# Kernel optimization log

Measured on AMD Instinct MI355X. Metric: run time of the kernel, lower is better.

## Reference

```python
import jax, jax.numpy as jnp
import numpy as np

N_QUBITS = 10
U3_LAYERS = 2
ENT_LAYERS = 2
EDGES = [[(q, (q + 1) % N_QUBITS) for q in range(N_QUBITS)] for _ in range(ENT_LAYERS)]
FIXED_W = [np.zeros(N_QUBITS, dtype=np.float32) for _ in range(ENT_LAYERS)]
C64 = jnp.complex64


def _rz(a):
    a = a.astype(C64)
    em, ep = jnp.exp(-0.5j * a), jnp.exp(0.5j * a)
    z = jnp.zeros((), C64)
    return jnp.stack([jnp.stack([em, z]), jnp.stack([z, ep])])


def _ry(t):
    c = jnp.cos(t / 2).astype(C64)
    s = jnp.sin(t / 2).astype(C64)
    return jnp.stack([jnp.stack([c, -s]), jnp.stack([s, c])])


def _rot(phi, theta, omega):
    # PennyLane Rot = RZ(omega) @ RY(theta) @ RZ(phi)
    return _rz(omega) @ _ry(theta) @ _rz(phi)


def _apply_1q(state, U, q):
    # state: (B,) + (2,)*n ; apply 2x2 U on qubit axis 1+q
    s = jnp.moveaxis(state, 1 + q, -1)
    s = s @ U.T
    return jnp.moveaxis(s, -1, 1 + q)


def _apply_cry(state, theta, u, v):
    U = _ry(theta)
    s = jnp.moveaxis(state, (1 + u, 1 + v), (-2, -1))  # (..., ctrl, tgt)
    c0 = s[..., 0, :]
    c1 = s[..., 1, :] @ U.T
    s = jnp.stack([c0, c1], axis=-2)
    return jnp.moveaxis(s, (-2, -1), (1 + u, 1 + v))


def _circuit(inputs, weights):
    B = inputs.shape[0]
    n = N_QUBITS
    # invert=True -> angles = pi * clamp(x, 0, 1)
    ang = jnp.pi * jnp.clip(inputs, 0.0, 1.0)
    # AngleEmbedding RY on |0...0> gives a product state
    c = jnp.cos(ang / 2).astype(C64)
    s = jnp.sin(ang / 2).astype(C64)
    st = jnp.ones((B, 1), C64)
    for q in range(n):
        amp = jnp.stack([c[:, q], s[:, q]], axis=-1)  # (B, 2)
        st = (st[:, :, None] * amp[:, None, :]).reshape(B, -1)
    st = st.reshape((B,) + (2,) * n)  # axis 1+q == wire q

    w_idx = 0
    for L in range(max(U3_LAYERS, ENT_LAYERS)):
        if L < U3_LAYERS:
            for q in range(n):
                U = _rot(weights[w_idx], weights[w_idx + 1], weights[w_idx + 2])
                w_idx += 3
                st = _apply_1q(st, U, q)
        if L < ENT_LAYERS:
            fw = FIXED_W[L]
            for i, (u, v) in enumerate(EDGES[L]):
                th = weights[w_idx] + fw[i]
                w_idx += 1
                st = _apply_cry(st, th, u, v)

    probs = (st.real ** 2 + st.imag ** 2)  # (B,) + (2,)*n
    outs = []
    for q in range(n):
        axes = tuple(a for a in range(1, n + 1) if a != 1 + q)
        m = jnp.sum(probs, axis=axes)  # (B, 2)
        outs.append(m[:, 0] - m[:, 1])
    return jnp.stack(outs, axis=-1)  # (B, n)


def setup_inputs() -> dict:
    key = jax.random.key(0)
    k1, k2 = jax.random.split(key)
    inputs = jax.random.uniform(k1, (8192, N_QUBITS), dtype=jnp.float32)
    weights = 0.1 * jax.random.normal(k2, (80,), dtype=jnp.float32)
    return {"inputs": inputs, "weights": weights}


def reference(inputs, weights):
    return _circuit(inputs, weights)
```

## Files before the change

kernel.cpp:

```cpp
#include <hip/hip_runtime.h>
#include <math.h>

#define NQ 10
typedef float v2f __attribute__((ext_vector_type(2)));

#define RL(v, l) __int_as_float(__builtin_amdgcn_readlane(__float_as_int(v), (l)))

template<int CTRL>
__device__ __forceinline__ float dppf(float x) {
    return __int_as_float(__builtin_amdgcn_update_dpp(
        __float_as_int(x), __float_as_int(x), CTRL, 0xF, 0xF, true));
}
template<int OFS>
__device__ __forceinline__ float swzf(float x) {
    return __int_as_float(__builtin_amdgcn_ds_swizzle(__float_as_int(x), OFS));
}
__device__ __forceinline__ float bperm(int idx, float x) {
    return __int_as_float(__builtin_amdgcn_ds_bpermute(idx, __float_as_int(x)));
}

template<int P>
__device__ __forceinline__ float partner1(float x, int bpx32) {
    if constexpr (P == 0) return dppf<0xB1>(x);
    else if constexpr (P == 1) return dppf<0x4E>(x);
    else if constexpr (P == 2) return swzf<0x101F>(x);
    else if constexpr (P == 3) return dppf<0x128>(x);
    else if constexpr (P == 4) return swzf<0x401F>(x);
    else return bperm(bpx32, x);
}
template<int P>
__device__ __forceinline__ v2f partner2(v2f v, int bpx32) {
    v2f r;
    r.x = partner1<P>(v.x, bpx32);
    r.y = partner1<P>(v.y, bpx32);
    return r;
}

__device__ __forceinline__ void u3_pair(v2f& a0r, v2f& a0i, v2f& a1r, v2f& a1i,
                                        float u00r, float u00i, float u01r, float u01i,
                                        float u10r, float u10i, float u11r, float u11i) {
    v2f n0r = u00r * a0r - u00i * a0i + u01r * a1r - u01i * a1i;
    v2f n0i = u00r * a0i + u00i * a0r + u01r * a1i + u01i * a1r;
    v2f n1r = u10r * a0r - u10i * a0i + u11r * a1r - u11i * a1i;
    v2f n1i = u10r * a0i + u10i * a0r + u11r * a1i + u11i * a1r;
    a0r = n0r; a0i = n0i; a1r = n1r; a1i = n1i;
}
__device__ __forceinline__ void ry_pair(v2f& a0r, v2f& a0i, v2f& a1r, v2f& a1i,
                                        float c, float s) {
    v2f n0r = c * a0r - s * a1r;
    v2f n0i = c * a0i - s * a1i;
    v2f n1r = s * a0r + c * a1r;
    v2f n1i = s * a0i + c * a1i;
    a0r = n0r; a0i = n0i; a1r = n1r; a1i = n1i;
}

template<int P>
__device__ __forceinline__ void u3_lane(v2f (&Sr)[8], v2f (&Si)[8], int lane, int bpx32,
                                        float u00r, float u00i, float u01r, float u01i,
                                        float u10r, float u10i, float u11r, float u11i) {
    const bool hi = (lane >> P) & 1;
    const float dr = hi ? u11r : u00r, di = hi ? u11i : u00i;
    const float orr = hi ? u10r : u01r, oii = hi ? u10i : u01i;
#pragma unroll
    for (int k = 0; k < 8; ++k) {
        const v2f mr = Sr[k], mi = Si[k];
        const v2f pr = partner2<P>(mr, bpx32);
        const v2f pi = partner2<P>(mi, bpx32);
        Sr[k] = dr * mr - di * mi + orr * pr - oii * pi;
        Si[k] = dr * mi + di * mr + orr * pi + oii * pr;
    }
}

template<int PC, int PT>
__device__ __forceinline__ void cry_lane(v2f (&Sr)[8], v2f (&Si)[8], int lane, int bpx32,
                                         float c, float s) {
    const bool ctrl = (lane >> PC) & 1;
    const float cl = ctrl ? c : 1.0f;
    const float sl = ctrl ? s : 0.0f;
    const bool hi = (lane >> PT) & 1;
    const float sgn = hi ? sl : -sl;
#pragma unroll
    for (int k = 0; k < 8; ++k) {
        const v2f pr = partner2<PT>(Sr[k], bpx32);
        const v2f pi = partner2<PT>(Si[k], bpx32);
        Sr[k] = cl * Sr[k] + sgn * pr;
        Si[k] = cl * Si[k] + sgn * pi;
    }
}

__device__ __forceinline__ float wave_sum(float x, int bpx32) {
    x += dppf<0xB1>(x);
    x += dppf<0x4E>(x);
    x += swzf<0x101F>(x);
    x += dppf<0x128>(x);
    x += swzf<0x401F>(x);
    x += bperm(bpx32, x);
    return x;
}

__global__ __launch_bounds__(256) void qsim(const float* __restrict__ in,
                                            const float* __restrict__ w,
                                            float* __restrict__ out, int B) {
    const int lane = threadIdx.x & 63;
    const int wave = threadIdx.x >> 6;
    int b = blockIdx.x * 4 + wave;
    b = __builtin_amdgcn_readfirstlane(b);
    if (b >= B) return;
    const int bpx32 = (lane ^ 32) << 2;

    float ang0 = 0.0f, ang1 = 0.0f, ang2 = 0.0f;
    if (lane < 20) {
        const int L = lane / 10, q = lane - L * 10;
        const int wi = L * 40 + q * 3;
        const float phi = w[wi], theta = w[wi + 1], omega = w[wi + 2];
        ang0 = 0.5f * theta;
        ang1 = 0.5f * (phi + omega);
        ang2 = 0.5f * (phi - omega);
    } else if (lane < 40) {
        const int g = lane - 20;
        const int L = g / 10, e = g - L * 10;
        ang0 = 0.5f * w[L * 40 + 30 + e];
    } else if (lane < 50) {
        float x = in[b * NQ + (lane - 40)];
        x = fminf(fmaxf(x, 0.0f), 1.0f);
        ang0 = 0.5f * 3.14159265358979323846f * x;
    }
    const float ca = __cosf(ang0), sa = __sinf(ang0);
    const float cb = __cosf(ang1), sb = __sinf(ang1);
    const float cg = __cosf(ang2), sg = __sinf(ang2);
    float c0, c1, c2, c3, c4, c5, c6, c7;
    c0 =  ca * cb;  c1 = -ca * sb;
    c2 = -sa * cg;  c3 = -sa * sg;
    c4 =  sa * cg;  c5 = -sa * sg;
    c6 =  ca * cb;  c7 =  ca * sb;
    if (lane >= 20) { c0 = ca; c1 = sa; }

#define U3C(L, q) \
    const float u00r = RL(c0, (L)*10+(q)), u00i = RL(c1, (L)*10+(q)), \
                u01r = RL(c2, (L)*10+(q)), u01i = RL(c3, (L)*10+(q)), \
                u10r = RL(c4, (L)*10+(q)), u10i = RL(c5, (L)*10+(q)), \
                u11r = RL(c6, (L)*10+(q)), u11i = RL(c7, (L)*10+(q));
#define CRYC(L, e) \
    const float c = RL(c0, 20+(L)*10+(e)), s = RL(c1, 20+(L)*10+(e));

    float cc[NQ], ss[NQ];
#pragma unroll
    for (int q = 0; q < NQ; ++q) { cc[q] = RL(c0, 40 + q); ss[q] = RL(c1, 40 + q); }
    float lamp = 1.0f;
#pragma unroll
    for (int j = 0; j < 6; ++j) lamp *= ((lane >> j) & 1) ? ss[9 - j] : cc[9 - j];

    v2f Sr[8], Si[8];
#pragma unroll
    for (int k = 0; k < 8; ++k) {
        float f = lamp;
        f *= (k & 1) ? ss[3] : cc[3];
        f *= (k & 2) ? ss[2] : cc[2];
        f *= (k & 4) ? ss[1] : cc[1];
        Sr[k] = (v2f){f * cc[0], f * ss[0]};
        Si[k] = (v2f){0.0f, 0.0f};
    }

#pragma unroll
    for (int L = 0; L < 2; ++L) {
        {
            U3C(L, 0);
            const v2f Dr = {u00r, u11r}, Di = {u00i, u11i};
            const v2f Or = {u01r, u10r}, Oi = {u01i, u10i};
#pragma unroll
            for (int k = 0; k < 8; ++k) {
                const v2f Ar = Sr[k], Ai = Si[k];
                const v2f Br = Ar.yx, Bi = Ai.yx;
                Sr[k] = Dr * Ar - Di * Ai + Or * Br - Oi * Bi;
                Si[k] = Dr * Ai + Di * Ar + Or * Bi + Oi * Br;
            }
        }
#pragma unroll
        for (int q = 1; q <= 3; ++q) {
            U3C(L, q);
            const int kb = (q == 1) ? 2 : (q == 2) ? 1 : 0;
            const int step = 1 << kb;
#pragma unroll
            for (int k0 = 0; k0 < 8; ++k0) {
                if (k0 & step) continue;
                const int k1 = k0 | step;
                u3_pair(Sr[k0], Si[k0], Sr[k1], Si[k1],
                        u00r, u00i, u01r, u01i, u10r, u10i, u11r, u11i);
            }
        }
        { U3C(L, 4); u3_lane<5>(Sr, Si, lane, bpx32, u00r,u00i,u01r,u01i,u10r,u10i,u11r,u11i); }
        { U3C(L, 5); u3_lane<4>(Sr, Si, lane, bpx32, u00r,u00i,u01r,u01i,u10r,u10i,u11r,u11i); }
        { U3C(L, 6); u3_lane<3>(Sr, Si, lane, bpx32, u00r,u00i,u01r,u01i,u10r,u10i,u11r,u11i); }
        { U3C(L, 7); u3_lane<2>(Sr, Si, lane, bpx32, u00r,u00i,u01r,u01i,u10r,u10i,u11r,u11i); }
        { U3C(L, 8); u3_lane<1>(Sr, Si, lane, bpx32, u00r,u00i,u01r,u01i,u10r,u10i,u11r,u11i); }
        { U3C(L, 9); u3_lane<0>(Sr, Si, lane, bpx32, u00r,u00i,u01r,u01i,u10r,u10i,u11r,u11i); }

        {
            CRYC(L, 0);
            const v2f cv = {1.0f, c};
            const v2f sv = {0.0f, s};
#pragma unroll
            for (int k0 = 0; k0 < 4; ++k0) {
                const int k1 = k0 | 4;
                v2f n0r = cv * Sr[k0] - sv * Sr[k1];
                v2f n0i = cv * Si[k0] - sv * Si[k1];
                v2f n1r = sv * Sr[k0] + cv * Sr[k1];
                v2f n1i = sv * Si[k0] + cv * Si[k1];
                Sr[k0] = n0r; Si[k0] = n0i; Sr[k1] = n1r; Si[k1] = n1i;
            }
        }
        {
            CRYC(L, 1);
            ry_pair(Sr[4], Si[4], Sr[6], Si[6], c, s);
            ry_pair(Sr[5], Si[5], Sr[7], Si[7], c, s);
        }
        {
            CRYC(L, 2);
            ry_pair(Sr[2], Si[2], Sr[3], Si[3], c, s);
            ry_pair(Sr[6], Si[6], Sr[7], Si[7], c, s);
        }
        {
            CRYC(L, 3);
            const bool hi = (lane >> 5) & 1;
            const float sgn = hi ? s : -s;
#pragma unroll
            for (int k = 1; k < 8; k += 2) {
                const v2f pr = partner2<5>(Sr[k], bpx32);
                const v2f pi = partner2<5>(Si[k], bpx32);
                Sr[k] = c * Sr[k] + sgn * pr;
                Si[k] = c * Si[k] + sgn * pi;
            }
        }
        { CRYC(L, 4); cry_lane<5, 4>(Sr, Si, lane, bpx32, c, s); }
        { CRYC(L, 5); cry_lane<4, 3>(Sr, Si, lane, bpx32, c, s); }
        { CRYC(L, 6); cry_lane<3, 2>(Sr, Si, lane, bpx32, c, s); }
        { CRYC(L, 7); cry_lane<2, 1>(Sr, Si, lane, bpx32, c, s); }
        { CRYC(L, 8); cry_lane<1, 0>(Sr, Si, lane, bpx32, c, s); }
        {
            CRYC(L, 9);
            const bool ctrl = lane & 1;
            const float cl = ctrl ? c : 1.0f;
            const float sl = ctrl ? s : 0.0f;
            const v2f C2 = {cl, cl};
            const v2f S2 = {-sl, sl};
#pragma unroll
            for (int k = 0; k < 8; ++k) {
                const v2f Ar = Sr[k], Ai = Si[k];
                Sr[k] = C2 * Ar + S2 * Ar.yx;
                Si[k] = C2 * Ai + S2 * Ai.yx;
            }
        }
    }

    v2f P[8];
    float ptot = 0.0f;
#pragma unroll
    for (int k = 0; k < 8; ++k) {
        P[k] = Sr[k] * Sr[k] + Si[k] * Si[k];
        ptot += P[k].x + P[k].y;
    }
    float z[NQ];
    {
        float acc = 0.0f;
#pragma unroll
        for (int k = 0; k < 8; ++k) acc += P[k].x - P[k].y;
        z[0] = acc;
    }
#pragma unroll
    for (int q = 1; q <= 3; ++q) {
        const int kb = (q == 1) ? 2 : (q == 2) ? 1 : 0;
        float acc = 0.0f;
#pragma unroll
        for (int k = 0; k < 8; ++k) {
            const float pk = P[k].x + P[k].y;
            acc += ((k >> kb) & 1) ? -pk : pk;
        }
        z[q] = acc;
    }
#pragma unroll
    for (int q = 4; q < NQ; ++q) {
        const int p = 9 - q;
        z[q] = ((lane >> p) & 1) ? -ptot : ptot;
    }
#pragma unroll
    for (int q = 0; q < NQ; ++q) z[q] = wave_sum(z[q], bpx32);

    if (lane == 0) {
#pragma unroll
        for (int q = 0; q < NQ; ++q) out[b * NQ + q] = z[q];
    }
}

extern "C" void kernel_launch(void* const* d_in, const int* in_sizes, int n_in,
                              void* d_out, int out_size, void* d_ws, size_t ws_size,
                              hipStream_t stream) {
    const float* inputs  = (const float*)d_in[0];
    const float* weights = (const float*)d_in[1];
    float* out = (float*)d_out;
    const int B = in_sizes[0] / NQ;

    qsim<<<(B + 3) / 4, 256, 0, stream>>>(inputs, weights, out, B);
}
```

Measured before the change: 96.66 us.

## Precompute fused gate matrices, fold embedding into first layer, use permlane swaps

A small precompute kernel builds the U3 matrices and fuses each CRY with the next U3 in the second layer into combined controlled matrices stored in workspace. The main kernel folds the embedding and first U3 layer into per-qubit single-qubit states, which removes the first-layer gate passes. Cross-half lane exchanges use permlane16/32 swap builtins when available. The Z-expectation reductions share a butterfly over the total probability. This adds a second kernel launch and workspace reads in exchange for fewer gate passes and fewer cross-lane ops.

Result: faster. 87.91 us (-9.0%).

```diff
diff --git a/kernel.cpp b/kernel.cpp
--- a/kernel.cpp
+++ b/kernel.cpp
@@ -4,7 +4,11 @@
 #define NQ 10
 typedef float v2f __attribute__((ext_vector_type(2)));
 
-#define RL(v, l) __int_as_float(__builtin_amdgcn_readlane(__float_as_int(v), (l)))
+#if defined(__has_builtin)
+#if __has_builtin(__builtin_amdgcn_permlane16_swap) && __has_builtin(__builtin_amdgcn_permlane32_swap)
+#define HAVE_PL 1
+#endif
+#endif
 
 template<int CTRL>
 __device__ __forceinline__ float dppf(float x) {
@@ -20,22 +24,100 @@
 }
 
 template<int P>
-__device__ __forceinline__ float partner1(float x, int bpx32) {
+__device__ __forceinline__ float partner1(float x) {
     if constexpr (P == 0) return dppf<0xB1>(x);
     else if constexpr (P == 1) return dppf<0x4E>(x);
     else if constexpr (P == 2) return swzf<0x101F>(x);
-    else if constexpr (P == 3) return dppf<0x128>(x);
-    else if constexpr (P == 4) return swzf<0x401F>(x);
-    else return bperm(bpx32, x);
-}
-template<int P>
-__device__ __forceinline__ v2f partner2(v2f v, int bpx32) {
-    v2f r;
-    r.x = partner1<P>(v.x, bpx32);
-    r.y = partner1<P>(v.y, bpx32);
-    return r;
-}
-
+    else return dppf<0x128>(x);
+}
+template<int P>
+__device__ __forceinline__ v2f partner2(v2f v) {
+    v2f r; r.x = partner1<P>(v.x); r.y = partner1<P>(v.y); return r;
+}
+
+struct FPair { float v0, v1; };
+template<int P>
+__device__ __forceinline__ FPair blkswap1(float x, int lane) {
+    FPair o;
+#ifdef HAVE_PL
+    if constexpr (P == 4) {
+        auto r = __builtin_amdgcn_permlane16_swap(__float_as_uint(x), __float_as_uint(x), false, false);
+        o.v0 = __uint_as_float(r[0]);
+        o.v1 = __uint_as_float(r[1]);
+    } else {
+        auto r = __builtin_amdgcn_permlane32_swap(__float_as_uint(x), __float_as_uint(x), false, false);
+        o.v0 = __uint_as_float(r[0]);
+        o.v1 = __uint_as_float(r[1]);
+    }
+#else
+    const float p = (P == 4) ? swzf<0x401F>(x) : bperm((lane ^ 32) << 2, x);
+    const bool hi = (lane >> P) & 1;
+    o.v0 = hi ? p : x;
+    o.v1 = hi ? x : p;
+#endif
+    return o;
+}
+struct VPair { v2f V0, V1; };
+template<int P>
+__device__ __forceinline__ VPair blkswap2(v2f x, int lane) {
+    const FPair a = blkswap1<P>(x.x, lane);
+    const FPair b = blkswap1<P>(x.y, lane);
+    VPair o;
+    o.V0 = (v2f){a.v0, b.v0};
+    o.V1 = (v2f){a.v1, b.v1};
+    return o;
+}
+template<int P>
+__device__ __forceinline__ float blkadd(float x, int lane) {
+    const FPair o = blkswap1<P>(x, lane);
+    return o.v0 + o.v1;
+}
+
+template<int P>
+__device__ __forceinline__ void gate_blk_full(v2f (&Sr)[8], v2f (&Si)[8], int lane,
+                                              float er, float ei, float fr, float fi) {
+#pragma unroll
+    for (int k = 0; k < 8; ++k) {
+        const VPair R = blkswap2<P>(Sr[k], lane);
+        const VPair I = blkswap2<P>(Si[k], lane);
+        Sr[k] = er * R.V0 - ei * I.V0 + fr * R.V1 - fi * I.V1;
+        Si[k] = er * I.V0 + ei * R.V0 + fr * I.V1 + fi * R.V1;
+    }
+}
+template<int P>
+__device__ __forceinline__ void gate_blk_real(v2f (&Sr)[8], v2f (&Si)[8], int lane,
+                                              float e, float f) {
+#pragma unroll
+    for (int k = 0; k < 8; ++k) {
+        const VPair R = blkswap2<P>(Sr[k], lane);
+        const VPair I = blkswap2<P>(Si[k], lane);
+        Sr[k] = e * R.V0 + f * R.V1;
+        Si[k] = e * I.V0 + f * I.V1;
+    }
+}
+template<int P>
+__device__ __forceinline__ void gate_dpp_full(v2f (&Sr)[8], v2f (&Si)[8],
+                                              float dr, float di, float orr, float oii) {
+#pragma unroll
+    for (int k = 0; k < 8; ++k) {
+        const v2f mr = Sr[k], mi = Si[k];
+        const v2f pr = partner2<P>(mr);
+        const v2f pi = partner2<P>(mi);
+        Sr[k] = dr * mr - di * mi + orr * pr - oii * pi;
+        Si[k] = dr * mi + di * mr + orr * pi + oii * pr;
+    }
+}
+template<int P>
+__device__ __forceinline__ void gate_dpp_real(v2f (&Sr)[8], v2f (&Si)[8],
+                                              float cl, float sgn) {
+#pragma unroll
+    for (int k = 0; k < 8; ++k) {
+        const v2f pr = partner2<P>(Sr[k]);
+        const v2f pi = partner2<P>(Si[k]);
+        Sr[k] = cl * Sr[k] + sgn * pr;
+        Si[k] = cl * Si[k] + sgn * pi;
+    }
+}
 __device__ __forceinline__ void u3_pair(v2f& a0r, v2f& a0i, v2f& a1r, v2f& a1i,
                                         float u00r, float u00i, float u01r, float u01i,
                                         float u10r, float u10i, float u11r, float u11i) {
@@ -53,237 +135,396 @@
     v2f n1i = s * a0i + c * a1i;
     a0r = n0r; a0i = n0i; a1r = n1r; a1i = n1i;
 }
-
-template<int P>
-__device__ __forceinline__ void u3_lane(v2f (&Sr)[8], v2f (&Si)[8], int lane, int bpx32,
-                                        float u00r, float u00i, float u01r, float u01i,
-                                        float u10r, float u10i, float u11r, float u11i) {
-    const bool hi = (lane >> P) & 1;
-    const float dr = hi ? u11r : u00r, di = hi ? u11i : u00i;
-    const float orr = hi ? u10r : u01r, oii = hi ? u10i : u01i;
-#pragma unroll
-    for (int k = 0; k < 8; ++k) {
-        const v2f mr = Sr[k], mi = Si[k];
-        const v2f pr = partner2<P>(mr, bpx32);
-        const v2f pi = partner2<P>(mi, bpx32);
-        Sr[k] = dr * mr - di * mi + orr * pr - oii * pi;
-        Si[k] = dr * mi + di * mr + orr * pi + oii * pr;
-    }
-}
-
-template<int PC, int PT>
-__device__ __forceinline__ void cry_lane(v2f (&Sr)[8], v2f (&Si)[8], int lane, int bpx32,
-                                         float c, float s) {
-    const bool ctrl = (lane >> PC) & 1;
-    const float cl = ctrl ? c : 1.0f;
-    const float sl = ctrl ? s : 0.0f;
-    const bool hi = (lane >> PT) & 1;
-    const float sgn = hi ? sl : -sl;
-#pragma unroll
-    for (int k = 0; k < 8; ++k) {
-        const v2f pr = partner2<PT>(Sr[k], bpx32);
-        const v2f pi = partner2<PT>(Si[k], bpx32);
-        Sr[k] = cl * Sr[k] + sgn * pr;
-        Si[k] = cl * Si[k] + sgn * pi;
-    }
-}
-
-__device__ __forceinline__ float wave_sum(float x, int bpx32) {
-    x += dppf<0xB1>(x);
-    x += dppf<0x4E>(x);
-    x += swzf<0x101F>(x);
-    x += dppf<0x128>(x);
-    x += swzf<0x401F>(x);
-    x += bperm(bpx32, x);
+__device__ __forceinline__ void cmul(float& xr, float& xi, float br, float bi) {
+    const float nr = xr * br - xi * bi;
+    const float ni = xr * bi + xi * br;
+    xr = nr; xi = ni;
+}
+
+template<int FROM>
+__device__ __forceinline__ float plus_reduce(float x, int lane) {
+    if constexpr (FROM <= 0) x += dppf<0xB1>(x);
+    if constexpr (FROM <= 1) x += dppf<0x4E>(x);
+    if constexpr (FROM <= 2) x += swzf<0x101F>(x);
+    if constexpr (FROM <= 3) x += dppf<0x128>(x);
+    if constexpr (FROM <= 4) x = blkadd<4>(x, lane);
+    x = blkadd<5>(x, lane);
     return x;
 }
 
+__device__ __forceinline__ void makeU3(float phi, float theta, float omega, float* u) {
+    const float ct = cosf(0.5f * theta), st = sinf(0.5f * theta);
+    const float apo = 0.5f * (phi + omega), amo = 0.5f * (phi - omega);
+    const float capo = cosf(apo), sapo = sinf(apo);
+    const float camo = cosf(amo), samo = sinf(amo);
+    u[0] =  capo * ct;  u[1] = -sapo * ct;
+    u[2] = -camo * st;  u[3] = -samo * st;
+    u[4] =  camo * st;  u[5] = -samo * st;
+    u[6] =  capo * ct;  u[7] =  sapo * ct;
+}
+
+__global__ void precompute(const float* __restrict__ w, float* __restrict__ cw) {
+    const int t = threadIdx.x;
+    if (t < 10) {
+        float u[8];
+        makeU3(w[t * 3], w[t * 3 + 1], w[t * 3 + 2], u);
+        float* p = cw + t * 8;
+        p[0] = u[0]; p[1] = u[2];
+        p[2] = u[1]; p[3] = u[3];
+        p[4] = u[4]; p[5] = u[6];
+        p[6] = u[5]; p[7] = u[7];
+    } else if (t < 20) {
+        const int q = t - 10;
+        float u[8];
+        makeU3(w[40 + q * 3], w[40 + q * 3 + 1], w[40 + q * 3 + 2], u);
+        float* p = cw + 100 + q * 8;
+        for (int i = 0; i < 8; ++i) p[i] = u[i];
+    } else if (t < 29) {
+        const int e = t - 20;
+        const float th = 0.5f * w[30 + e];
+        cw[80 + 2 * e] = cosf(th);
+        cw[81 + 2 * e] = sinf(th);
+    } else if (t == 29) {
+        const float th = 0.5f * w[79];
+        cw[98] = cosf(th);
+        cw[99] = sinf(th);
+    } else if (t < 40) {
+        const int q = t - 30;
+        float u[8];
+        makeU3(w[40 + q * 3], w[40 + q * 3 + 1], w[40 + q * 3 + 2], u);
+        float* p = cw + 180 + q * 8;
+        if (q == 0) {
+            const float th = 0.5f * w[39];
+            const float ct = cosf(th), st = sinf(th);
+            p[0] = u[0] * ct + u[2] * st;  p[1] = u[1] * ct + u[3] * st;
+            p[2] = u[2] * ct - u[0] * st;  p[3] = u[3] * ct - u[1] * st;
+            p[4] = u[4] * ct + u[6] * st;  p[5] = u[5] * ct + u[7] * st;
+            p[6] = u[6] * ct - u[4] * st;  p[7] = u[7] * ct - u[5] * st;
+        } else {
+            const float th = 0.5f * w[70 + (q - 1)];
+            const float ct = cosf(th), st = sinf(th);
+            p[0] = ct * u[0] - st * u[4];  p[1] = ct * u[1] - st * u[5];
+            p[2] = ct * u[2] - st * u[6];  p[3] = ct * u[3] - st * u[7];
+            p[4] = st * u[0] + ct * u[4];  p[5] = st * u[1] + ct * u[5];
+            p[6] = st * u[2] + ct * u[6];  p[7] = st * u[3] + ct * u[7];
+        }
+    }
+}
+
+#define LOADM(P, base) \
+    const float P##00r = cf[(base) + 0], P##00i = cf[(base) + 1], \
+                P##01r = cf[(base) + 2], P##01i = cf[(base) + 3], \
+                P##10r = cf[(base) + 4], P##10i = cf[(base) + 5], \
+                P##11r = cf[(base) + 6], P##11i = cf[(base) + 7];
+
 __global__ __launch_bounds__(256) void qsim(const float* __restrict__ in,
-                                            const float* __restrict__ w,
+                                            const float* __restrict__ cf,
                                             float* __restrict__ out, int B) {
+    __shared__ float tsh[4 * 40];
     const int lane = threadIdx.x & 63;
     const int wave = threadIdx.x >> 6;
     int b = blockIdx.x * 4 + wave;
     b = __builtin_amdgcn_readfirstlane(b);
     if (b >= B) return;
-    const int bpx32 = (lane ^ 32) << 2;
-
-    float ang0 = 0.0f, ang1 = 0.0f, ang2 = 0.0f;
-    if (lane < 20) {
-        const int L = lane / 10, q = lane - L * 10;
-        const int wi = L * 40 + q * 3;
-        const float phi = w[wi], theta = w[wi + 1], omega = w[wi + 2];
-        ang0 = 0.5f * theta;
-        ang1 = 0.5f * (phi + omega);
-        ang2 = 0.5f * (phi - omega);
-    } else if (lane < 40) {
-        const int g = lane - 20;
-        const int L = g / 10, e = g - L * 10;
-        ang0 = 0.5f * w[L * 40 + 30 + e];
-    } else if (lane < 50) {
-        float x = in[b * NQ + (lane - 40)];
+
+    if (lane < 40) {
+        const int q = lane >> 2;
+        float x = in[b * NQ + q];
         x = fminf(fmaxf(x, 0.0f), 1.0f);
-        ang0 = 0.5f * 3.14159265358979323846f * x;
-    }
-    const float ca = __cosf(ang0), sa = __sinf(ang0);
-    const float cb = __cosf(ang1), sb = __sinf(ang1);
-    const float cg = __cosf(ang2), sg = __sinf(ang2);
-    float c0, c1, c2, c3, c4, c5, c6, c7;
-    c0 =  ca * cb;  c1 = -ca * sb;
-    c2 = -sa * cg;  c3 = -sa * sg;
-    c4 =  sa * cg;  c5 = -sa * sg;
-    c6 =  ca * cb;  c7 =  ca * sb;
-    if (lane >= 20) { c0 = ca; c1 = sa; }
-
-#define U3C(L, q) \
-    const float u00r = RL(c0, (L)*10+(q)), u00i = RL(c1, (L)*10+(q)), \
-                u01r = RL(c2, (L)*10+(q)), u01i = RL(c3, (L)*10+(q)), \
-                u10r = RL(c4, (L)*10+(q)), u10i = RL(c5, (L)*10+(q)), \
-                u11r = RL(c6, (L)*10+(q)), u11i = RL(c7, (L)*10+(q));
-#define CRYC(L, e) \
-    const float c = RL(c0, 20+(L)*10+(e)), s = RL(c1, 20+(L)*10+(e));
-
-    float cc[NQ], ss[NQ];
-#pragma unroll
-    for (int q = 0; q < NQ; ++q) { cc[q] = RL(c0, 40 + q); ss[q] = RL(c1, 40 + q); }
-    float lamp = 1.0f;
-#pragma unroll
-    for (int j = 0; j < 6; ++j) lamp *= ((lane >> j) & 1) ? ss[9 - j] : cc[9 - j];
-
+        const float a = 0.5f * 3.14159265358979323846f * x;
+        const float ca = __cosf(a), sa = __sinf(a);
+        const float M0 = cf[lane * 2], M1 = cf[lane * 2 + 1];
+        tsh[wave * 40 + lane] = M0 * ca + M1 * sa;
+    }
+    const int base = wave * 40;
+
+    float wr, wi;
+    {
+        const int bit = lane & 1;
+        const float2 v = *(const float2*)&tsh[base + 9 * 4 + (bit << 1)];
+        wr = v.x; wi = v.y;
+    }
+#pragma unroll
+    for (int j = 1; j < 6; ++j) {
+        const int bit = (lane >> j) & 1;
+        const float2 v = *(const float2*)&tsh[base + (9 - j) * 4 + (bit << 1)];
+        cmul(wr, wi, v.x, v.y);
+    }
+    const float4 T0 = *(const float4*)&tsh[base + 0];
+    const float4 T1 = *(const float4*)&tsh[base + 4];
+    const float4 T2 = *(const float4*)&tsh[base + 8];
+    const float4 T3 = *(const float4*)&tsh[base + 12];
+
+    float vr[4], vi[4];
+    { float r = T1.x, i2 = T1.y; vr[0] = r * T2.x - i2 * T2.y; vi[0] = r * T2.y + i2 * T2.x;
+                                  vr[1] = r * T2.z - i2 * T2.w; vi[1] = r * T2.w + i2 * T2.z; }
+    { float r = T1.z, i2 = T1.w; vr[2] = r * T2.x - i2 * T2.y; vi[2] = r * T2.y + i2 * T2.x;
+                                  vr[3] = r * T2.z - i2 * T2.w; vi[3] = r * T2.w + i2 * T2.z; }
     v2f Sr[8], Si[8];
+    const v2f T0r = {T0.x, T0.z};
+    const v2f T0i = {T0.y, T0.w};
 #pragma unroll
     for (int k = 0; k < 8; ++k) {
-        float f = lamp;
-        f *= (k & 1) ? ss[3] : cc[3];
-        f *= (k & 2) ? ss[2] : cc[2];
-        f *= (k & 4) ? ss[1] : cc[1];
-        Sr[k] = (v2f){f * cc[0], f * ss[0]};
-        Si[k] = (v2f){0.0f, 0.0f};
-    }
-
-#pragma unroll
-    for (int L = 0; L < 2; ++L) {
-        {
-            U3C(L, 0);
-            const v2f Dr = {u00r, u11r}, Di = {u00i, u11i};
-            const v2f Or = {u01r, u10r}, Oi = {u01i, u10i};
-#pragma unroll
-            for (int k = 0; k < 8; ++k) {
-                const v2f Ar = Sr[k], Ai = Si[k];
-                const v2f Br = Ar.yx, Bi = Ai.yx;
-                Sr[k] = Dr * Ar - Di * Ai + Or * Br - Oi * Bi;
-                Si[k] = Dr * Ai + Di * Ar + Or * Bi + Oi * Br;
-            }
-        }
-#pragma unroll
-        for (int q = 1; q <= 3; ++q) {
-            U3C(L, q);
-            const int kb = (q == 1) ? 2 : (q == 2) ? 1 : 0;
-            const int step = 1 << kb;
-#pragma unroll
-            for (int k0 = 0; k0 < 8; ++k0) {
-                if (k0 & step) continue;
-                const int k1 = k0 | step;
-                u3_pair(Sr[k0], Si[k0], Sr[k1], Si[k1],
-                        u00r, u00i, u01r, u01i, u10r, u10i, u11r, u11i);
-            }
-        }
-        { U3C(L, 4); u3_lane<5>(Sr, Si, lane, bpx32, u00r,u00i,u01r,u01i,u10r,u10i,u11r,u11i); }
-        { U3C(L, 5); u3_lane<4>(Sr, Si, lane, bpx32, u00r,u00i,u01r,u01i,u10r,u10i,u11r,u11i); }
-        { U3C(L, 6); u3_lane<3>(Sr, Si, lane, bpx32, u00r,u00i,u01r,u01i,u10r,u10i,u11r,u11i); }
-        { U3C(L, 7); u3_lane<2>(Sr, Si, lane, bpx32, u00r,u00i,u01r,u01i,u10r,u10i,u11r,u11i); }
-        { U3C(L, 8); u3_lane<1>(Sr, Si, lane, bpx32, u00r,u00i,u01r,u01i,u10r,u10i,u11r,u11i); }
-        { U3C(L, 9); u3_lane<0>(Sr, Si, lane, bpx32, u00r,u00i,u01r,u01i,u10r,u10i,u11r,u11i); }
-
-        {
-            CRYC(L, 0);
-            const v2f cv = {1.0f, c};
-            const v2f sv = {0.0f, s};
-#pragma unroll
-            for (int k0 = 0; k0 < 4; ++k0) {
-                const int k1 = k0 | 4;
-                v2f n0r = cv * Sr[k0] - sv * Sr[k1];
-                v2f n0i = cv * Si[k0] - sv * Si[k1];
-                v2f n1r = sv * Sr[k0] + cv * Sr[k1];
-                v2f n1i = sv * Si[k0] + cv * Si[k1];
-                Sr[k0] = n0r; Si[k0] = n0i; Sr[k1] = n1r; Si[k1] = n1i;
-            }
-        }
-        {
-            CRYC(L, 1);
-            ry_pair(Sr[4], Si[4], Sr[6], Si[6], c, s);
-            ry_pair(Sr[5], Si[5], Sr[7], Si[7], c, s);
-        }
-        {
-            CRYC(L, 2);
-            ry_pair(Sr[2], Si[2], Sr[3], Si[3], c, s);
-            ry_pair(Sr[6], Si[6], Sr[7], Si[7], c, s);
-        }
-        {
-            CRYC(L, 3);
-            const bool hi = (lane >> 5) & 1;
-            const float sgn = hi ? s : -s;
-#pragma unroll
-            for (int k = 1; k < 8; k += 2) {
-                const v2f pr = partner2<5>(Sr[k], bpx32);
-                const v2f pi = partner2<5>(Si[k], bpx32);
-                Sr[k] = c * Sr[k] + sgn * pr;
-                Si[k] = c * Si[k] + sgn * pi;
-            }
-        }
-        { CRYC(L, 4); cry_lane<5, 4>(Sr, Si, lane, bpx32, c, s); }
-        { CRYC(L, 5); cry_lane<4, 3>(Sr, Si, lane, bpx32, c, s); }
-        { CRYC(L, 6); cry_lane<3, 2>(Sr, Si, lane, bpx32, c, s); }
-        { CRYC(L, 7); cry_lane<2, 1>(Sr, Si, lane, bpx32, c, s); }
-        { CRYC(L, 8); cry_lane<1, 0>(Sr, Si, lane, bpx32, c, s); }
-        {
-            CRYC(L, 9);
-            const bool ctrl = lane & 1;
-            const float cl = ctrl ? c : 1.0f;
-            const float sl = ctrl ? s : 0.0f;
-            const v2f C2 = {cl, cl};
-            const v2f S2 = {-sl, sl};
-#pragma unroll
-            for (int k = 0; k < 8; ++k) {
-                const v2f Ar = Sr[k], Ai = Si[k];
-                Sr[k] = C2 * Ar + S2 * Ar.yx;
-                Si[k] = C2 * Ai + S2 * Ai.yx;
-            }
+        const int hv = k >> 1;
+        const float t3r = (k & 1) ? T3.z : T3.x;
+        const float t3i = (k & 1) ? T3.w : T3.y;
+        float kr = vr[hv] * t3r - vi[hv] * t3i;
+        float ki = vr[hv] * t3i + vi[hv] * t3r;
+        cmul(kr, ki, wr, wi);
+        Sr[k] = kr * T0r - ki * T0i;
+        Si[k] = kr * T0i + ki * T0r;
+    }
+
+    {
+        const float c = cf[80], s = cf[81];
+        const v2f cv = {1.0f, c};
+        const v2f sv = {0.0f, s};
+#pragma unroll
+        for (int k0 = 0; k0 < 4; ++k0) {
+            const int k1 = k0 | 4;
+            v2f n0r = cv * Sr[k0] - sv * Sr[k1];
+            v2f n0i = cv * Si[k0] - sv * Si[k1];
+            v2f n1r = sv * Sr[k0] + cv * Sr[k1];
+            v2f n1i = sv * Si[k0] + cv * Si[k1];
+            Sr[k0] = n0r; Si[k0] = n0i; Sr[k1] = n1r; Si[k1] = n1i;
+        }
+    }
+    {
+        const float c = cf[82], s = cf[83];
+        ry_pair(Sr[4], Si[4], Sr[6], Si[6], c, s);
+        ry_pair(Sr[5], Si[5], Sr[7], Si[7], c, s);
+    }
+    {
+        const float c = cf[84], s = cf[85];
+        ry_pair(Sr[2], Si[2], Sr[3], Si[3], c, s);
+        ry_pair(Sr[6], Si[6], Sr[7], Si[7], c, s);
+    }
+    {
+        const float c = cf[86], s = cf[87];
+        const bool hi = (lane >> 5) & 1;
+        const float e = hi ? s : c;
+        const float f = hi ? c : -s;
+#pragma unroll
+        for (int k = 1; k < 8; k += 2) {
+            const VPair R = blkswap2<5>(Sr[k], lane);
+            const VPair I = blkswap2<5>(Si[k], lane);
+            Sr[k] = e * R.V0 + f * R.V1;
+            Si[k] = e * I.V0 + f * I.V1;
+        }
+    }
+    {
+        const float c = cf[88], s = cf[89];
+        const bool ctrl = (lane >> 5) & 1;
+        const bool hi = (lane >> 4) & 1;
+        const float e = ctrl ? (hi ? s : c) : (hi ? 0.0f : 1.0f);
+        const float f = ctrl ? (hi ? c : -s) : (hi ? 1.0f : 0.0f);
+        gate_blk_real<4>(Sr, Si, lane, e, f);
+    }
+    {
+        const float c = cf[90], s = cf[91];
+        const bool ctrl = (lane >> 4) & 1;
+        const float cl = ctrl ? c : 1.0f;
+        const float sl = ctrl ? s : 0.0f;
+        const float sgn = ((lane >> 3) & 1) ? sl : -sl;
+        gate_dpp_real<3>(Sr, Si, cl, sgn);
+    }
+    {
+        const float c = cf[92], s = cf[93];
+        const bool ctrl = (lane >> 3) & 1;
+        const float cl = ctrl ? c : 1.0f;
+        const float sl = ctrl ? s : 0.0f;
+        const float sgn = ((lane >> 2) & 1) ? sl : -sl;
+        gate_dpp_real<2>(Sr, Si, cl, sgn);
+    }
+    {
+        const float c = cf[94], s = cf[95];
+        const bool ctrl = (lane >> 2) & 1;
+        const float cl = ctrl ? c : 1.0f;
+        const float sl = ctrl ? s : 0.0f;
+        const float sgn = ((lane >> 1) & 1) ? sl : -sl;
+        gate_dpp_real<1>(Sr, Si, cl, sgn);
+    }
+    {
+        const float c = cf[96], s = cf[97];
+        const bool ctrl = (lane >> 1) & 1;
+        const float cl = ctrl ? c : 1.0f;
+        const float sl = ctrl ? s : 0.0f;
+        const float sgn = (lane & 1) ? sl : -sl;
+        gate_dpp_real<0>(Sr, Si, cl, sgn);
+    }
+
+    {
+        LOADM(A, 100); LOADM(Bm, 180);
+        const bool ctrl = lane & 1;
+        const float M00r = ctrl ? Bm00r : A00r, M00i = ctrl ? Bm00i : A00i;
+        const float M01r = ctrl ? Bm01r : A01r, M01i = ctrl ? Bm01i : A01i;
+        const float M10r = ctrl ? Bm10r : A10r, M10i = ctrl ? Bm10i : A10i;
+        const float M11r = ctrl ? Bm11r : A11r, M11i = ctrl ? Bm11i : A11i;
+        const v2f Dr = {M00r, M11r}, Di = {M00i, M11i};
+        const v2f Or = {M01r, M10r}, Oi = {M01i, M10i};
+#pragma unroll
+        for (int k = 0; k < 8; ++k) {
+            const v2f Ar = Sr[k], Ai = Si[k];
+            const v2f Br = Ar.yx, Bi = Ai.yx;
+            Sr[k] = Dr * Ar - Di * Ai + Or * Br - Oi * Bi;
+            Si[k] = Dr * Ai + Di * Ar + Or * Bi + Oi * Br;
+        }
+    }
+    {
+        LOADM(A, 108); LOADM(Bm, 188);
+        const v2f u00r = {A00r, Bm00r}, u00i = {A00i, Bm00i};
+        const v2f u01r = {A01r, Bm01r}, u01i = {A01i, Bm01i};
+        const v2f u10r = {A10r, Bm10r}, u10i = {A10i, Bm10i};
+        const v2f u11r = {A11r, Bm11r}, u11i = {A11i, Bm11i};
+#pragma unroll
+        for (int k0 = 0; k0 < 4; ++k0) {
+            const int k1 = k0 | 4;
+            v2f n0r = u00r * Sr[k0] - u00i * Si[k0] + u01r * Sr[k1] - u01i * Si[k1];
+            v2f n0i = u00r * Si[k0] + u00i * Sr[k0] + u01r * Si[k1] + u01i * Sr[k1];
+            v2f n1r = u10r * Sr[k0] - u10i * Si[k0] + u11r * Sr[k1] - u11i * Si[k1];
+            v2f n1i = u10r * Si[k0] + u10i * Sr[k0] + u11r * Si[k1] + u11i * Sr[k1];
+            Sr[k0] = n0r; Si[k0] = n0i; Sr[k1] = n1r; Si[k1] = n1i;
+        }
+    }
+    {
+        LOADM(A, 116); LOADM(Bm, 196);
+        u3_pair(Sr[0], Si[0], Sr[2], Si[2], A00r, A00i, A01r, A01i, A10r, A10i, A11r, A11i);
+        u3_pair(Sr[1], Si[1], Sr[3], Si[3], A00r, A00i, A01r, A01i, A10r, A10i, A11r, A11i);
+        u3_pair(Sr[4], Si[4], Sr[6], Si[6], Bm00r, Bm00i, Bm01r, Bm01i, Bm10r, Bm10i, Bm11r, Bm11i);
+        u3_pair(Sr[5], Si[5], Sr[7], Si[7], Bm00r, Bm00i, Bm01r, Bm01i, Bm10r, Bm10i, Bm11r, Bm11i);
+    }
+    {
+        LOADM(A, 124); LOADM(Bm, 204);
+        u3_pair(Sr[0], Si[0], Sr[1], Si[1], A00r, A00i, A01r, A01i, A10r, A10i, A11r, A11i);
+        u3_pair(Sr[4], Si[4], Sr[5], Si[5], A00r, A00i, A01r, A01i, A10r, A10i, A11r, A11i);
+        u3_pair(Sr[2], Si[2], Sr[3], Si[3], Bm00r, Bm00i, Bm01r, Bm01i, Bm10r, Bm10i, Bm11r, Bm11i);
+        u3_pair(Sr[6], Si[6], Sr[7], Si[7], Bm00r, Bm00i, Bm01r, Bm01i, Bm10r, Bm10i, Bm11r, Bm11i);
+    }
+    {
+        LOADM(A, 132); LOADM(Bm, 212);
+        const bool hi = (lane >> 5) & 1;
+        const float eAr = hi ? A10r : A00r, eAi = hi ? A10i : A00i;
+        const float fAr = hi ? A11r : A01r, fAi = hi ? A11i : A01i;
+        const float eBr = hi ? Bm10r : Bm00r, eBi = hi ? Bm10i : Bm00i;
+        const float fBr = hi ? Bm11r : Bm01r, fBi = hi ? Bm11i : Bm01i;
+#pragma unroll
+        for (int k = 0; k < 8; ++k) {
+            const float er = (k & 1) ? eBr : eAr, ei = (k & 1) ? eBi : eAi;
+            const float fr = (k & 1) ? fBr : fAr, fi = (k & 1) ? fBi : fAi;
+            const VPair R = blkswap2<5>(Sr[k], lane);
+            const VPair I = blkswap2<5>(Si[k], lane);
+            Sr[k] = er * R.V0 - ei * I.V0 + fr * R.V1 - fi * I.V1;
+            Si[k] = er * I.V0 + ei * R.V0 + fr * I.V1 + fi * R.V1;
+        }
+    }
+    {
+        LOADM(A, 140); LOADM(Bm, 220);
+        const bool ctrl = (lane >> 5) & 1;
+        const bool hi = (lane >> 4) & 1;
+        const float M00r = ctrl ? Bm00r : A00r, M00i = ctrl ? Bm00i : A00i;
+        const float M01r = ctrl ? Bm01r : A01r, M01i = ctrl ? Bm01i : A01i;
+        const float M10r = ctrl ? Bm10r : A10r, M10i = ctrl ? Bm10i : A10i;
+        const float M11r = ctrl ? Bm11r : A11r, M11i = ctrl ? Bm11i : A11i;
+        const float er = hi ? M10r : M00r, ei = hi ? M10i : M00i;
+        const float fr = hi ? M11r : M01r, fi = hi ? M11i : M01i;
+        gate_blk_full<4>(Sr, Si, lane, er, ei, fr, fi);
+    }
+    {
+        LOADM(A, 148); LOADM(Bm, 228);
+        const bool ctrl = (lane >> 4) & 1;
+        const bool hi = (lane >> 3) & 1;
+        const float M00r = ctrl ? Bm00r : A00r, M00i = ctrl ? Bm00i : A00i;
+        const float M01r = ctrl ? Bm01r : A01r, M01i = ctrl ? Bm01i : A01i;
+        const float M10r = ctrl ? Bm10r : A10r, M10i = ctrl ? Bm10i : A10i;
+        const float M11r = ctrl ? Bm11r : A11r, M11i = ctrl ? Bm11i : A11i;
+        const float dr = hi ? M11r : M00r, di = hi ? M11i : M00i;
+        const float orr = hi ? M10r : M01r, oii = hi ? M10i : M01i;
+        gate_dpp_full<3>(Sr, Si, dr, di, orr, oii);
+    }
+    {
+        LOADM(A, 156); LOADM(Bm, 236);
+        const bool ctrl = (lane >> 3) & 1;
+        const bool hi = (lane >> 2) & 1;
+        const float M00r = ctrl ? Bm00r : A00r, M00i = ctrl ? Bm00i : A00i;
+        const float M01r = ctrl ? Bm01r : A01r, M01i = ctrl ? Bm01i : A01i;
+        const float M10r = ctrl ? Bm10r : A10r, M10i = ctrl ? Bm10i : A10i;
+        const float M11r = ctrl ? Bm11r : A11r, M11i = ctrl ? Bm11i : A11i;
+        const float dr = hi ? M11r : M00r, di = hi ? M11i : M00i;
+        const float orr = hi ? M10r : M01r, oii = hi ? M10i : M01i;
+        gate_dpp_full<2>(Sr, Si, dr, di, orr, oii);
+    }
+    {
+        LOADM(A, 164); LOADM(Bm, 244);
+        const bool ctrl = (lane >> 2) & 1;
+        const bool hi = (lane >> 1) & 1;
+        const float M00r = ctrl ? Bm00r : A00r, M00i = ctrl ? Bm00i : A00i;
+        const float M01r = ctrl ? Bm01r : A01r, M01i = ctrl ? Bm01i : A01i;
+        const float M10r = ctrl ? Bm10r : A10r, M10i = ctrl ? Bm10i : A10i;
+        const float M11r = ctrl ? Bm11r : A11r, M11i = ctrl ? Bm11i : A11i;
+        const float dr = hi ? M11r : M00r, di = hi ? M11i : M00i;
+        const float orr = hi ? M10r : M01r, oii = hi ? M10i : M01i;
+        gate_dpp_full<1>(Sr, Si, dr, di, orr, oii);
+    }
+    {
+        LOADM(A, 172); LOADM(Bm, 252);
+        const bool ctrl = (lane >> 1) & 1;
+        const bool hi = lane & 1;
+        const float M00r = ctrl ? Bm00r : A00r, M00i = ctrl ? Bm00i : A00i;
+        const float M01r = ctrl ? Bm01r : A01r, M01i = ctrl ? Bm01i : A01i;
+        const float M10r = ctrl ? Bm10r : A10r, M10i = ctrl ? Bm10i : A10i;
+        const float M11r = ctrl ? Bm11r : A11r, M11i = ctrl ? Bm11i : A11i;
+        const float dr = hi ? M11r : M00r, di = hi ? M11i : M00i;
+        const float orr = hi ? M10r : M01r, oii = hi ? M10i : M01i;
+        gate_dpp_full<0>(Sr, Si, dr, di, orr, oii);
+    }
+    {
+        const float c = cf[98], s = cf[99];
+        const bool ctrl = lane & 1;
+        const float cl = ctrl ? c : 1.0f;
+        const float sl = ctrl ? s : 0.0f;
+        const v2f C2 = {cl, cl};
+        const v2f S2 = {-sl, sl};
+#pragma unroll
+        for (int k = 0; k < 8; ++k) {
+            const v2f Ar = Sr[k], Ai = Si[k];
+            Sr[k] = C2 * Ar + S2 * Ar.yx;
+            Si[k] = C2 * Ai + S2 * Ai.yx;
         }
     }
 
     v2f P[8];
-    float ptot = 0.0f;
+    float ptot = 0.0f, z0p = 0.0f, z1p = 0.0f, z2p = 0.0f, z3p = 0.0f;
 #pragma unroll
     for (int k = 0; k < 8; ++k) {
         P[k] = Sr[k] * Sr[k] + Si[k] * Si[k];
-        ptot += P[k].x + P[k].y;
+        const float sk = P[k].x + P[k].y;
+        ptot += sk;
+        z0p += P[k].x - P[k].y;
+        z1p += ((k >> 2) & 1) ? -sk : sk;
+        z2p += ((k >> 1) & 1) ? -sk : sk;
+        z3p += (k & 1) ? -sk : sk;
+    }
+    float d0, d1, d2, d3, d4, d5;
+    {
+        float a = ptot, p;
+        p = dppf<0xB1>(a);   d0 = a - p; a += p;
+        p = dppf<0x4E>(a);   d1 = a - p; a += p;
+        p = swzf<0x101F>(a); d2 = a - p; a += p;
+        p = dppf<0x128>(a);  d3 = a - p; a += p;
+        { const FPair o = blkswap1<4>(a, lane); d4 = o.v0 - o.v1; a = o.v0 + o.v1; }
+        { const FPair o = blkswap1<5>(a, lane); d5 = o.v0 - o.v1; }
     }
     float z[NQ];
-    {
-        float acc = 0.0f;
-#pragma unroll
-        for (int k = 0; k < 8; ++k) acc += P[k].x - P[k].y;
-        z[0] = acc;
-    }
-#pragma unroll
-    for (int q = 1; q <= 3; ++q) {
-        const int kb = (q == 1) ? 2 : (q == 2) ? 1 : 0;
-        float acc = 0.0f;
-#pragma unroll
-        for (int k = 0; k < 8; ++k) {
-            const float pk = P[k].x + P[k].y;
-            acc += ((k >> kb) & 1) ? -pk : pk;
-        }
-        z[q] = acc;
-    }
-#pragma unroll
-    for (int q = 4; q < NQ; ++q) {
-        const int p = 9 - q;
-        z[q] = ((lane >> p) & 1) ? -ptot : ptot;
-    }
-#pragma unroll
-    for (int q = 0; q < NQ; ++q) z[q] = wave_sum(z[q], bpx32);
+    z[0] = plus_reduce<0>(z0p, lane);
+    z[1] = plus_reduce<0>(z1p, lane);
+    z[2] = plus_reduce<0>(z2p, lane);
+    z[3] = plus_reduce<0>(z3p, lane);
+    z[4] = d5;
+    z[5] = plus_reduce<5>(d4, lane);
+    z[6] = plus_reduce<4>(d3, lane);
+    z[7] = plus_reduce<3>(d2, lane);
+    z[8] = plus_reduce<2>(d1, lane);
+    z[9] = plus_reduce<1>(d0, lane);
 
     if (lane == 0) {
 #pragma unroll
@@ -297,7 +538,9 @@
     const float* inputs  = (const float*)d_in[0];
     const float* weights = (const float*)d_in[1];
     float* out = (float*)d_out;
+    float* cw  = (float*)d_ws;
     const int B = in_sizes[0] / NQ;
 
-    qsim<<<(B + 3) / 4, 256, 0, stream>>>(inputs, weights, out, B);
-}
+    precompute<<<1, 64, 0, stream>>>(weights, cw);
+    qsim<<<(B + 3) / 4, 256, 0, stream>>>(inputs, cw, out, B);
+}
```
